# Performance work log

Measured on AMD Instinct MI355X. Metric: run time of the kernel, lower is better.

## Reference

```python
import jax, jax.numpy as jnp
import numpy as np

B, S, E, H = 2, 2048, 1024, 16
D = E // H  # head_dim = 64


def setup_inputs() -> dict:
    key = jax.random.key(0)
    ks = jax.random.split(key, 7)
    scale = 1.0 / np.sqrt(E)
    return {
        "q": jax.random.normal(ks[0], (B, S, E), jnp.float32),
        "k": jax.random.normal(ks[1], (B, S, E), jnp.float32),
        "v": jax.random.normal(ks[2], (B, S, E), jnp.float32),
        "Wq": jax.random.normal(ks[3], (E, E), jnp.float32) * scale,
        "bq": jnp.zeros((E,), jnp.float32),
        "Wk": jax.random.normal(ks[4], (E, E), jnp.float32) * scale,
        "bk": jnp.zeros((E,), jnp.float32),
        "Wv": jax.random.normal(ks[5], (E, E), jnp.float32) * scale,
        "bv": jnp.zeros((E,), jnp.float32),
        "Wo": jax.random.normal(ks[6], (E, E), jnp.float32) * scale,
        "bo": jnp.zeros((E,), jnp.float32),
    }


def _split_heads(x):
    # [B, S, E] -> [B, H, S, D]
    b, s, _ = x.shape
    return x.reshape(b, s, H, D).transpose(0, 2, 1, 3)


def reference(q, k, v, Wq, bq, Wk, bk, Wv, bv, Wo, bo):
    qh = _split_heads(q @ Wq + bq)  # [B,H,S,D]
    kh = _split_heads(k @ Wk + bk)
    vh = _split_heads(v @ Wv + bv)
    scores = jnp.einsum("bhqd,bhkd->bhqk", qh, kh) / jnp.sqrt(jnp.float32(D))
    # causal mask, TF band_part(ones, -1, 0) == lower triangular
    mask = jnp.tril(jnp.ones((S, S), jnp.float32))
    scores = scores * mask - 1e9 * (1.0 - mask)
    weights = jax.nn.softmax(scores, axis=-1)
    attn = jnp.einsum("bhqk,bhkd->bhqd", weights, vh)  # [B,H,S,D]
    concat = attn.transpose(0, 2, 1, 3).reshape(q.shape[0], S, E)
    return concat @ Wo + bo
```

## Files before the change

kernel.cpp:

```cpp
#include <hip/hip_runtime.h>
#include <math.h>

#define Bd 2
#define Sd 2048
#define Ed 1024
#define Hd 16
#define Dd 64
#define Md (Bd * Sd)
#define Kd 1024
#define Nd 1024

typedef __attribute__((ext_vector_type(8))) short bf16x8;
typedef __attribute__((ext_vector_type(4))) float f32x4;

__device__ __forceinline__ unsigned short f2bf(float f) {
    unsigned x = __float_as_uint(f);
    x += 0x7fffu + ((x >> 16) & 1u);
    return (unsigned short)(x >> 16);
}

__device__ __forceinline__ unsigned pk_bf16_rhu(float a, float b) {
    return __builtin_amdgcn_perm(__float_as_uint(b) + 0x8000u,
                                 __float_as_uint(a) + 0x8000u, 0x07060302u);
}

__device__ __forceinline__ void gl2lds16(const unsigned short* g, unsigned short* l) {
    __builtin_amdgcn_global_load_lds(
        (__attribute__((address_space(1))) void*)g,
        (__attribute__((address_space(3))) void*)l, 16, 0, 0);
}

__global__ __launch_bounds__(256) void prep_k(
    const float* __restrict__ q, const float* __restrict__ k, const float* __restrict__ v,
    unsigned short* __restrict__ qb, unsigned short* __restrict__ kb,
    unsigned short* __restrict__ vb,
    const float* __restrict__ w0, const float* __restrict__ w1,
    const float* __restrict__ w2, const float* __restrict__ w3,
    unsigned short* __restrict__ o0, unsigned short* __restrict__ o1,
    unsigned short* __restrict__ o2, unsigned short* __restrict__ o3)
{
    const int bx = blockIdx.x;
    if (bx < 3072) {
        const int zz = bx >> 10;
        const int blk = bx & 1023;
        const float* s = zz == 0 ? q : zz == 1 ? k : v;
        unsigned short* d = zz == 0 ? qb : zz == 1 ? kb : vb;
        const int n4 = (Bd * Sd * Ed) / 4;
        int i = blk * 256 + threadIdx.x;
        for (; i < n4; i += 1024 * 256) {
            float4 x = ((const float4*)s)[i];
            uint2 u = make_uint2(pk_bf16_rhu(x.x, x.y), pk_bf16_rhu(x.z, x.w));
            ((uint2*)d)[i] = u;
        }
        return;
    }
    __shared__ unsigned short Tl[32][36];
    const int idx = bx - 3072;
    const int z   = idx >> 10;
    const int ky  = (idx >> 5) & 31;
    const int nx  = idx & 31;
    const float* W = z == 0 ? w0 : z == 1 ? w1 : z == 2 ? w2 : w3;
    unsigned short* Wt = z == 0 ? o0 : z == 1 ? o1 : z == 2 ? o2 : o3;

    const int t = threadIdx.x;
    const int r = t >> 3;
    const int c4 = (t & 7) * 4;
    const int k0 = ky * 32;
    const int n0 = nx * 32;

    float4 x = *(const float4*)(W + (size_t)(k0 + r) * Nd + n0 + c4);
    Tl[c4 + 0][r] = f2bf(x.x);
    Tl[c4 + 1][r] = f2bf(x.y);
    Tl[c4 + 2][r] = f2bf(x.z);
    Tl[c4 + 3][r] = f2bf(x.w);
    __syncthreads();
    ushort4 u = make_ushort4(Tl[r][c4 + 0], Tl[r][c4 + 1], Tl[r][c4 + 2], Tl[r][c4 + 3]);
    *(ushort4*)(Wt + (size_t)(n0 + r) * Kd + k0 + c4) = u;
}

template <int AM>
__device__ __forceinline__ void gemm_v5(
    const unsigned short* __restrict__ A, const unsigned short* __restrict__ Bt,
    const float* __restrict__ bias, void* __restrict__ Yv,
    int m0, int n0, int mode, float oscale)
{
    constexpr int AMT = AM / 32;
    __shared__ unsigned short As[2][AM * 32];
    __shared__ unsigned short Bs[2][128 * 32];

    const int tid  = threadIdx.x;
    const int w    = tid >> 6;
    const int lane = tid & 63;
    const int ln   = lane & 15;
    const int quad = lane >> 4;
    const int wm = (w >> 1) * (AM / 2);
    const int wn = (w & 1) * 64;

    const int lrow = lane >> 2;
    const int lcol = (lane & 3) * 8;

    const unsigned short* Bg0 = Bt + (size_t)(n0 + (2 * w) * 16 + lrow) * Kd + lcol;
    const unsigned short* Bg1 = Bg0 + 16 * Kd;
    const int aseg = (AM == 128) ? 2 * w : w;
    const unsigned short* Ag0 = A + (size_t)(m0 + aseg * 16 + lrow) * Kd + lcol;
    const unsigned short* Ag1 = Ag0 + 16 * Kd;

    f32x4 acc[AMT][4];
    #pragma unroll
    for (int i = 0; i < AMT; ++i)
        #pragma unroll
        for (int j = 0; j < 4; ++j)
            acc[i][j] = (f32x4){0.f, 0.f, 0.f, 0.f};

    gl2lds16(Bg0, &Bs[0][(2 * w) * 512]);
    gl2lds16(Bg1, &Bs[0][(2 * w) * 512 + 512]);
    gl2lds16(Ag0, &As[0][aseg * 512]);
    if constexpr (AM == 128) gl2lds16(Ag1, &As[0][aseg * 512 + 512]);

    for (int k0 = 0; k0 < Kd; k0 += 32) {
        const int buf = (k0 >> 5) & 1;
        __syncthreads();

        if (k0 + 32 < Kd) {
            gl2lds16(Bg0 + k0 + 32, &Bs[buf ^ 1][(2 * w) * 512]);
            gl2lds16(Bg1 + k0 + 32, &Bs[buf ^ 1][(2 * w) * 512 + 512]);
            gl2lds16(Ag0 + k0 + 32, &As[buf ^ 1][aseg * 512]);
            if constexpr (AM == 128)
                gl2lds16(Ag1 + k0 + 32, &As[buf ^ 1][aseg * 512 + 512]);
        }

        bf16x8 af[AMT], bfr[4];
        #pragma unroll
        for (int mi = 0; mi < AMT; ++mi)
            af[mi] = *(const bf16x8*)(&As[buf][(wm + mi * 16 + ln) * 32 + quad * 8]);
        #pragma unroll
        for (int ni = 0; ni < 4; ++ni)
            bfr[ni] = *(const bf16x8*)(&Bs[buf][(wn + ni * 16 + ln) * 32 + quad * 8]);
        #pragma unroll
        for (int mi = 0; mi < AMT; ++mi)
            #pragma unroll
            for (int ni = 0; ni < 4; ++ni)
                acc[mi][ni] = __builtin_amdgcn_mfma_f32_16x16x32_bf16(
                    af[mi], bfr[ni], acc[mi][ni], 0, 0, 0);
    }

    float bval[4];
    #pragma unroll
    for (int ni = 0; ni < 4; ++ni) bval[ni] = bias[n0 + wn + ni * 16 + ln];

    if (mode == 0) {
        float* Y = (float*)Yv;
        #pragma unroll
        for (int mi = 0; mi < AMT; ++mi) {
            #pragma unroll
            for (int ni = 0; ni < 4; ++ni) {
                int n = n0 + wn + ni * 16 + ln;
                #pragma unroll
                for (int r = 0; r < 4; ++r) {
                    int m = m0 + wm + mi * 16 + quad * 4 + r;
                    Y[(size_t)m * Nd + n] = (acc[mi][ni][r] + bval[ni]) * oscale;
                }
            }
        }
    } else if (mode == 1) {
        unsigned short* Y = (unsigned short*)Yv;
        #pragma unroll
        for (int mi = 0; mi < AMT; ++mi) {
            #pragma unroll
            for (int ni = 0; ni < 4; ++ni) {
                int n = n0 + wn + ni * 16 + ln;
                int h = n >> 6, d = n & 63;
                #pragma unroll
                for (int r = 0; r < 4; ++r) {
                    int m = m0 + wm + mi * 16 + quad * 4 + r;
                    int b = m >> 11, s = m & 2047;
                    Y[(((size_t)b * Hd + h) * Sd + s) * Dd + d] =
                        f2bf((acc[mi][ni][r] + bval[ni]) * oscale);
                }
            }
        }
    } else {
        unsigned short* Y = (unsigned short*)Yv;
        #pragma unroll
        for (int mi = 0; mi < AMT; ++mi) {
            int mbase = m0 + wm + mi * 16 + quad * 4;
            int b = mbase >> 11, s = mbase & 2047;
            #pragma unroll
            for (int ni = 0; ni < 4; ++ni) {
                int n = n0 + wn + ni * 16 + ln;
                int h = n >> 6, d = n & 63;
                ushort4 u = make_ushort4(
                    f2bf((acc[mi][ni][0] + bval[ni]) * oscale),
                    f2bf((acc[mi][ni][1] + bval[ni]) * oscale),
                    f2bf((acc[mi][ni][2] + bval[ni]) * oscale),
                    f2bf((acc[mi][ni][3] + bval[ni]) * oscale));
                *(ushort4*)(Y + (((size_t)b * Hd + h) * Dd + d) * Sd + s) = u;
            }
        }
    }
}

__global__ __launch_bounds__(256) void proj_gemm_k(
    const unsigned short* A0, const unsigned short* A1, const unsigned short* A2,
    const unsigned short* B0, const unsigned short* B1, const unsigned short* B2,
    const float* b0, const float* b1, const float* b2,
    unsigned short* Y0, unsigned short* Y1, unsigned short* Y2)
{
    const int l    = blockIdx.x;
    const int xcd  = l & 7;
    const int g    = l >> 3;
    const int n_t  = g & 7;
    const int msub = (g >> 3) & 3;
    const int z    = g >> 5;
    const int m_t  = xcd * 4 + msub;

    const unsigned short* A = z == 0 ? A0 : z == 1 ? A1 : A2;
    const unsigned short* B = z == 0 ? B0 : z == 1 ? B1 : B2;
    const float* bias       = z == 0 ? b0 : z == 1 ? b1 : b2;
    unsigned short* Y       = z == 0 ? Y0 : z == 1 ? Y1 : Y2;
    gemm_v5<128>(A, B, bias, Y, m_t * 128, n_t * 128,
                 z == 2 ? 2 : 1,
                 z == 0 ? 0.18033688011112042f : 1.0f);
}

__global__ __launch_bounds__(256) void out_gemm_k(
    const unsigned short* A, const unsigned short* Bt, const float* bias, float* Y)
{
    const int l    = blockIdx.x;
    const int xcd  = l & 7;
    const int g    = l >> 3;
    const int n_t  = g & 7;
    const int msub = g >> 3;
    const int m_t  = xcd * 8 + msub;
    gemm_v5<64>(A, Bt, bias, Y, m_t * 64, n_t * 128, 0, 1.0f);
}

__global__ __launch_bounds__(256) void attn_mfma_k(
    const unsigned short* __restrict__ Qg,
    const unsigned short* __restrict__ Kg,
    const unsigned short* __restrict__ Vg,
    unsigned short* __restrict__ Aout)
{
    __shared__ unsigned short Ks[2][2][64 * 64];
    __shared__ unsigned short Vs[2][2][64 * 64];
    __shared__ unsigned short Pt[4][16][72];

    const int tid  = threadIdx.x;
    const int w    = tid >> 6;
    const int lane = tid & 63;
    const int ln   = lane & 15;
    const int quad = lane >> 4;

    const int l   = blockIdx.x;
    const int bh  = (l & 7) * 4 + ((l >> 3) & 3);
    const int qtA = l >> 5;
    const int qtB = 31 - qtA;
    const int b   = bh >> 4;
    const int h   = bh & 15;

    const size_t baseQK = (size_t)bh * Sd * Dd;
    const size_t baseV  = (size_t)bh * Dd * Sd;
    const f32x4 vzero = {0.f, 0.f, 0.f, 0.f};

    const int nsub = qtB + 1;
    const int ngrp = (nsub + 1) >> 1;

    const int sr = lane >> 3;
    const int sc = ((lane & 7) ^ sr) * 8;
    const int rb0 = w * 16, rb1 = w * 16 + 8;
    const int swl = ln & 7;
    const int c0 = ((quad    ) ^ swl) * 8;
    const int c1 = ((quad + 4) ^ swl) * 8;

    const int qrowA = qtA * 64 + w * 16;
    const int qrowB = qtB * 64 + w * 16;
    const int qgA = qrowA + ln, qgB = qrowB + ln;
    const unsigned short* qpA = Qg + baseQK + (size_t)qgA * Dd + 8 * quad;
    const unsigned short* qpB = Qg + baseQK + (size_t)qgB * Dd + 8 * quad;
    const bf16x8 qA0 = *(const bf16x8*)(qpA), qA1 = *(const bf16x8*)(qpA + 32);
    const bf16x8 qB0 = *(const bf16x8*)(qpB), qB1 = *(const bf16x8*)(qpB + 32);

    float lA = 0.f, lB = 0.f;
    f32x4 OA[4], OB[4];
    #pragma unroll
    for (int t = 0; t < 4; ++t) { OA[t] = vzero; OB[t] = vzero; }

    const unsigned short* Kst0 = Kg + baseQK + (size_t)(rb0 + sr) * Dd + sc;
    const unsigned short* Kst1 = Kg + baseQK + (size_t)(rb1 + sr) * Dd + sc;
    const unsigned short* Vst0 = Vg + baseV  + (size_t)(rb0 + sr) * Sd + sc;
    const unsigned short* Vst1 = Vg + baseV  + (size_t)(rb1 + sr) * Sd + sc;

    #pragma unroll
    for (int s = 0; s < 2; ++s) {
        const int nk = s * 64;
        gl2lds16(Kst0 + (size_t)nk * Dd, &Ks[0][s][rb0 * 64]);
        gl2lds16(Kst1 + (size_t)nk * Dd, &Ks[0][s][rb1 * 64]);
        gl2lds16(Vst0 + nk, &Vs[0][s][rb0 * 64]);
        gl2lds16(Vst1 + nk, &Vs[0][s][rb1 * 64]);
    }

    for (int g = 0; g < ngrp; ++g) {
        const int cur = g & 1;
        __syncthreads();

        if (g + 1 < ngrp) {
            #pragma unroll
            for (int s = 0; s < 2; ++s) {
                const int ts = 2 * (g + 1) + s;
                if (ts < nsub) {
                    const int nk = ts * 64;
                    gl2lds16(Kst0 + (size_t)nk * Dd, &Ks[cur ^ 1][s][rb0 * 64]);
                    gl2lds16(Kst1 + (size_t)nk * Dd, &Ks[cur ^ 1][s][rb1 * 64]);
                    gl2lds16(Vst0 + nk, &Vs[cur ^ 1][s][rb0 * 64]);
                    gl2lds16(Vst1 + nk, &Vs[cur ^ 1][s][rb1 * 64]);
                }
            }
        }

        #pragma unroll
        for (int s = 0; s < 2; ++s) {
            const int it = 2 * g + s;
            if (it >= nsub) break;
            const int nk  = it * 64;
            const bool doA = (it <= qtA);

            bf16x8 kf0[4], kf1[4];
            #pragma unroll
            for (int t = 0; t < 4; ++t) {
                const int R = (t * 16 + ln) * 64;
                kf0[t] = *(const bf16x8*)&Ks[cur][s][R + c0];
                kf1[t] = *(const bf16x8*)&Ks[cur][s][R + c1];
            }

            f32x4 SB[4], SA[4];
            #pragma unroll
            for (int t = 0; t < 4; ++t) {
                f32x4 z = __builtin_amdgcn_mfma_f32_16x16x32_bf16(kf0[t], qB0, vzero, 0, 0, 0);
                SB[t]   = __builtin_amdgcn_mfma_f32_16x16x32_bf16(kf1[t], qB1, z,     0, 0, 0);
            }
            if (doA) {
                #pragma unroll
                for (int t = 0; t < 4; ++t) {
                    f32x4 z = __builtin_amdgcn_mfma_f32_16x16x32_bf16(kf0[t], qA0, vzero, 0, 0, 0);
                    SA[t]   = __builtin_amdgcn_mfma_f32_16x16x32_bf16(kf1[t], qA1, z,     0, 0, 0);
                }
            }

            if (it == qtB) {
                #pragma unroll
                for (int t = 0; t < 4; ++t)
                    #pragma unroll
                    for (int r = 0; r < 4; ++r)
                        if (nk + t * 16 + quad * 4 + r > qgB)
                            SB[t][r] = -1e30f;
            }
            if (doA && it == qtA) {
                #pragma unroll
                for (int t = 0; t < 4; ++t)
                    #pragma unroll
                    for (int r = 0; r < 4; ++r)
                        if (nk + t * 16 + quad * 4 + r > qgA)
                            SA[t][r] = -1e30f;
            }

            {
                float p[16]; float rsum = 0.f;
                #pragma unroll
                for (int t = 0; t < 4; ++t)
                    #pragma unroll
                    for (int r = 0; r < 4; ++r) {
                        float e = __builtin_amdgcn_exp2f(SB[t][r]);
                        p[t * 4 + r] = e; rsum += e;
                    }
                lB += rsum;
                #pragma unroll
                for (int t = 0; t < 4; ++t) {
                    uint2 u = make_uint2(pk_bf16_rhu(p[t * 4 + 0], p[t * 4 + 1]),
                                         pk_bf16_rhu(p[t * 4 + 2], p[t * 4 + 3]));
                    *(uint2*)&Pt[w][ln][t * 16 + quad * 4] = u;
                }
            }
            const bf16x8 pfB0 = *(const bf16x8*)&Pt[w][ln][8 * quad];
            const bf16x8 pfB1 = *(const bf16x8*)&Pt[w][ln][32 + 8 * quad];

            bf16x8 pfA0, pfA1;
            if (doA) {
                float p[16]; float rsum = 0.f;
                #pragma unroll
                for (int t = 0; t < 4; ++t)
                    #pragma unroll
                    for (int r = 0; r < 4; ++r) {
                        float e = __builtin_amdgcn_exp2f(SA[t][r]);
                        p[t * 4 + r] = e; rsum += e;
                    }
                lA += rsum;
                #pragma unroll
                for (int t = 0; t < 4; ++t) {
                    uint2 u = make_uint2(pk_bf16_rhu(p[t * 4 + 0], p[t * 4 + 1]),
                                         pk_bf16_rhu(p[t * 4 + 2], p[t * 4 + 3]));
                    *(uint2*)&Pt[w][ln][t * 16 + quad * 4] = u;
                }
                pfA0 = *(const bf16x8*)&Pt[w][ln][8 * quad];
                pfA1 = *(const bf16x8*)&Pt[w][ln][32 + 8 * quad];
            }

            #pragma unroll
            for (int t = 0; t < 4; ++t) {
                const int R = (t * 16 + ln) * 64;
                bf16x8 v0 = *(const bf16x8*)&Vs[cur][s][R + c0];
                bf16x8 v1 = *(const bf16x8*)&Vs[cur][s][R + c1];
                OB[t] = __builtin_amdgcn_mfma_f32_16x16x32_bf16(v0, pfB0, OB[t], 0, 0, 0);
                OB[t] = __builtin_amdgcn_mfma_f32_16x16x32_bf16(v1, pfB1, OB[t], 0, 0, 0);
                if (doA) {
                    OA[t] = __builtin_amdgcn_mfma_f32_16x16x32_bf16(v0, pfA0, OA[t], 0, 0, 0);
                    OA[t] = __builtin_amdgcn_mfma_f32_16x16x32_bf16(v1, pfA1, OA[t], 0, 0, 0);
                }
            }

            if (doA && it == qtA) {
                float l_run = lA;
                l_run += __shfl_xor(l_run, 16);
                l_run += __shfl_xor(l_run, 32);
                float inv = 1.f / l_run;
                unsigned short* op =
                    Aout + ((size_t)b * Sd + qgA) * Ed + h * 64 + quad * 4;
                #pragma unroll
                for (int t = 0; t < 4; ++t) {
                    ushort4 u = make_ushort4(f2bf(OA[t][0] * inv), f2bf(OA[t][1] * inv),
                                             f2bf(OA[t][2] * inv), f2bf(OA[t][3] * inv));
                    *(ushort4*)(op + t * 16) = u;
                }
            }
        }
    }

    float l_run = lB;
    l_run += __shfl_xor(l_run, 16);
    l_run += __shfl_xor(l_run, 32);
    float inv = 1.f / l_run;
    unsigned short* op = Aout + ((size_t)b * Sd + qgB) * Ed + h * 64 + quad * 4;
    #pragma unroll
    for (int t = 0; t < 4; ++t) {
        ushort4 u = make_ushort4(f2bf(OB[t][0] * inv), f2bf(OB[t][1] * inv),
                                 f2bf(OB[t][2] * inv), f2bf(OB[t][3] * inv));
        *(ushort4*)(op + t * 16) = u;
    }
}

extern "C" void kernel_launch(void* const* d_in, const int* in_sizes, int n_in,
                              void* d_out, int out_size, void* d_ws, size_t ws_size,
                              hipStream_t stream) {
    const float* q  = (const float*)d_in[0];
    const float* k  = (const float*)d_in[1];
    const float* v  = (const float*)d_in[2];
    const float* Wq = (const float*)d_in[3];
    const float* bq = (const float*)d_in[4];
    const float* Wk = (const float*)d_in[5];
    const float* bk = (const float*)d_in[6];
    const float* Wv = (const float*)d_in[7];
    const float* bv = (const float*)d_in[8];
    const float* Wo = (const float*)d_in[9];
    const float* bo = (const float*)d_in[10];

    const size_t TENS = (size_t)Bd * Sd * Ed;
    const size_t WE   = (size_t)Ed * Ed;
    unsigned short* qb  = (unsigned short*)d_ws;
    unsigned short* kb  = qb + TENS;
    unsigned short* vb  = kb + TENS;
    unsigned short* Wqt = vb + TENS;
    unsigned short* Wkt = Wqt + WE;
    unsigned short* Wvt = Wkt + WE;
    unsigned short* Wot = Wvt + WE;
    unsigned short* Qh  = Wot + WE;
    unsigned short* Kh  = Qh + TENS;
    unsigned short* Vt  = Kh + TENS;
    unsigned short* An  = Vt + TENS;

    prep_k<<<dim3(7168), 256, 0, stream>>>(q, k, v, qb, kb, vb,
                                           Wq, Wk, Wv, Wo, Wqt, Wkt, Wvt, Wot);
    proj_gemm_k<<<dim3(768), 256, 0, stream>>>(
        qb, kb, vb, Wqt, Wkt, Wvt, bq, bk, bv, Qh, Kh, Vt);
    attn_mfma_k<<<dim3(512), 256, 0, stream>>>(Qh, Kh, Vt, An);
    out_gemm_k<<<dim3(512), 256, 0, stream>>>(An, Wot, bo, (float*)d_out);
}
```

Before: 208.0 us.

## Split attention KV sub-tiles across two wave groups with LDS merge

```diff
diff --git a/kernel.cpp b/kernel.cpp
--- a/kernel.cpp
+++ b/kernel.cpp
@@ -235,18 +235,21 @@
     gemm_v5<64>(A, Bt, bias, Y, m_t * 64, n_t * 128, 0, 1.0f);
 }
 
-__global__ __launch_bounds__(256) void attn_mfma_k(
+__global__ __launch_bounds__(512, 4) void attn_mfma_k(
     const unsigned short* __restrict__ Qg,
     const unsigned short* __restrict__ Kg,
     const unsigned short* __restrict__ Vg,
     unsigned short* __restrict__ Aout)
 {
-    __shared__ unsigned short Ks[2][2][64 * 64];
-    __shared__ unsigned short Vs[2][2][64 * 64];
-    __shared__ unsigned short Pt[4][16][72];
+    __shared__ unsigned short lds_all[40960];
+    unsigned short* Ksb = lds_all;
+    unsigned short* Vsb = lds_all + 16384;
+    unsigned short* Ptb = lds_all + 32768;
 
     const int tid  = threadIdx.x;
-    const int w    = tid >> 6;
+    const int w8   = tid >> 6;
+    const int grp  = w8 >> 2;
+    const int w    = w8 & 3;
     const int lane = tid & 63;
     const int ln   = lane & 15;
     const int quad = lane >> 4;
@@ -265,12 +268,13 @@
     const int nsub = qtB + 1;
     const int ngrp = (nsub + 1) >> 1;
 
+    const int rw = w8 * 8;
     const int sr = lane >> 3;
     const int sc = ((lane & 7) ^ sr) * 8;
-    const int rb0 = w * 16, rb1 = w * 16 + 8;
     const int swl = ln & 7;
     const int c0 = ((quad    ) ^ swl) * 8;
     const int c1 = ((quad + 4) ^ swl) * 8;
+    const int pswz = swl << 3;
 
     const int qrowA = qtA * 64 + w * 16;
     const int qrowB = qtB * 64 + w * 16;
@@ -285,18 +289,15 @@
     #pragma unroll
     for (int t = 0; t < 4; ++t) { OA[t] = vzero; OB[t] = vzero; }
 
-    const unsigned short* Kst0 = Kg + baseQK + (size_t)(rb0 + sr) * Dd + sc;
-    const unsigned short* Kst1 = Kg + baseQK + (size_t)(rb1 + sr) * Dd + sc;
-    const unsigned short* Vst0 = Vg + baseV  + (size_t)(rb0 + sr) * Sd + sc;
-    const unsigned short* Vst1 = Vg + baseV  + (size_t)(rb1 + sr) * Sd + sc;
+    const unsigned short* Kst = Kg + baseQK + (size_t)(rw + sr) * Dd + sc;
+    const unsigned short* Vst = Vg + baseV  + (size_t)(rw + sr) * Sd + sc;
+    unsigned short* Ptw = Ptb + (w8 * 16 + ln) * 64;
 
     #pragma unroll
     for (int s = 0; s < 2; ++s) {
         const int nk = s * 64;
-        gl2lds16(Kst0 + (size_t)nk * Dd, &Ks[0][s][rb0 * 64]);
-        gl2lds16(Kst1 + (size_t)nk * Dd, &Ks[0][s][rb1 * 64]);
-        gl2lds16(Vst0 + nk, &Vs[0][s][rb0 * 64]);
-        gl2lds16(Vst1 + nk, &Vs[0][s][rb1 * 64]);
+        gl2lds16(Kst + (size_t)nk * Dd, Ksb + s * 4096 + rw * 64);
+        gl2lds16(Vst + nk,              Vsb + s * 4096 + rw * 64);
     }
 
     for (int g = 0; g < ngrp; ++g) {
@@ -309,27 +310,27 @@
                 const int ts = 2 * (g + 1) + s;
                 if (ts < nsub) {
                     const int nk = ts * 64;
-                    gl2lds16(Kst0 + (size_t)nk * Dd, &Ks[cur ^ 1][s][rb0 * 64]);
-                    gl2lds16(Kst1 + (size_t)nk * Dd, &Ks[cur ^ 1][s][rb1 * 64]);
-                    gl2lds16(Vst0 + nk, &Vs[cur ^ 1][s][rb0 * 64]);
-                    gl2lds16(Vst1 + nk, &Vs[cur ^ 1][s][rb1 * 64]);
-                }
-            }
-        }
-
-        #pragma unroll
-        for (int s = 0; s < 2; ++s) {
-            const int it = 2 * g + s;
-            if (it >= nsub) break;
+                    gl2lds16(Kst + (size_t)nk * Dd,
+                             Ksb + ((cur ^ 1) * 2 + s) * 4096 + rw * 64);
+                    gl2lds16(Vst + nk,
+                             Vsb + ((cur ^ 1) * 2 + s) * 4096 + rw * 64);
+                }
+            }
+        }
+
+        const int it = 2 * g + grp;
+        if (it < nsub) {
             const int nk  = it * 64;
             const bool doA = (it <= qtA);
+            const unsigned short* Kc = Ksb + (cur * 2 + grp) * 4096;
+            const unsigned short* Vc = Vsb + (cur * 2 + grp) * 4096;
 
             bf16x8 kf0[4], kf1[4];
             #pragma unroll
             for (int t = 0; t < 4; ++t) {
                 const int R = (t * 16 + ln) * 64;
-                kf0[t] = *(const bf16x8*)&Ks[cur][s][R + c0];
-                kf1[t] = *(const bf16x8*)&Ks[cur][s][R + c1];
+                kf0[t] = *(const bf16x8*)&Kc[R + c0];
+                kf1[t] = *(const bf16x8*)&Kc[R + c1];
             }
 
             f32x4 SB[4], SA[4];
@@ -377,11 +378,11 @@
                 for (int t = 0; t < 4; ++t) {
                     uint2 u = make_uint2(pk_bf16_rhu(p[t * 4 + 0], p[t * 4 + 1]),
                                          pk_bf16_rhu(p[t * 4 + 2], p[t * 4 + 3]));
-                    *(uint2*)&Pt[w][ln][t * 16 + quad * 4] = u;
-                }
-            }
-            const bf16x8 pfB0 = *(const bf16x8*)&Pt[w][ln][8 * quad];
-            const bf16x8 pfB1 = *(const bf16x8*)&Pt[w][ln][32 + 8 * quad];
+                    *(uint2*)&Ptw[(t * 16 + quad * 4) ^ pswz] = u;
+                }
+            }
+            const bf16x8 pfB0 = *(const bf16x8*)&Ptw[(8 * quad) ^ pswz];
+            const bf16x8 pfB1 = *(const bf16x8*)&Ptw[(32 + 8 * quad) ^ pswz];
 
             bf16x8 pfA0, pfA1;
             if (doA) {
@@ -398,17 +399,17 @@
                 for (int t = 0; t < 4; ++t) {
                     uint2 u = make_uint2(pk_bf16_rhu(p[t * 4 + 0], p[t * 4 + 1]),
                                          pk_bf16_rhu(p[t * 4 + 2], p[t * 4 + 3]));
-                    *(uint2*)&Pt[w][ln][t * 16 + quad * 4] = u;
-                }
-                pfA0 = *(const bf16x8*)&Pt[w][ln][8 * quad];
-                pfA1 = *(const bf16x8*)&Pt[w][ln][32 + 8 * quad];
+                    *(uint2*)&Ptw[(t * 16 + quad * 4) ^ pswz] = u;
+                }
+                pfA0 = *(const bf16x8*)&Ptw[(8 * quad) ^ pswz];
+                pfA1 = *(const bf16x8*)&Ptw[(32 + 8 * quad) ^ pswz];
             }
 
             #pragma unroll
             for (int t = 0; t < 4; ++t) {
                 const int R = (t * 16 + ln) * 64;
-                bf16x8 v0 = *(const bf16x8*)&Vs[cur][s][R + c0];
-                bf16x8 v1 = *(const bf16x8*)&Vs[cur][s][R + c1];
+                bf16x8 v0 = *(const bf16x8*)&Vc[R + c0];
+                bf16x8 v1 = *(const bf16x8*)&Vc[R + c1];
                 OB[t] = __builtin_amdgcn_mfma_f32_16x16x32_bf16(v0, pfB0, OB[t], 0, 0, 0);
                 OB[t] = __builtin_amdgcn_mfma_f32_16x16x32_bf16(v1, pfB1, OB[t], 0, 0, 0);
                 if (doA) {
@@ -416,34 +417,54 @@
                     OA[t] = __builtin_amdgcn_mfma_f32_16x16x32_bf16(v1, pfA1, OA[t], 0, 0, 0);
                 }
             }
-
-            if (doA && it == qtA) {
-                float l_run = lA;
-                l_run += __shfl_xor(l_run, 16);
-                l_run += __shfl_xor(l_run, 32);
-                float inv = 1.f / l_run;
-                unsigned short* op =
-                    Aout + ((size_t)b * Sd + qgA) * Ed + h * 64 + quad * 4;
-                #pragma unroll
-                for (int t = 0; t < 4; ++t) {
-                    ushort4 u = make_ushort4(f2bf(OA[t][0] * inv), f2bf(OA[t][1] * inv),
-                                             f2bf(OA[t][2] * inv), f2bf(OA[t][3] * inv));
-                    *(ushort4*)(op + t * 16) = u;
-                }
-            }
-        }
-    }
-
-    float l_run = lB;
-    l_run += __shfl_xor(l_run, 16);
-    l_run += __shfl_xor(l_run, 32);
-    float inv = 1.f / l_run;
-    unsigned short* op = Aout + ((size_t)b * Sd + qgB) * Ed + h * 64 + quad * 4;
-    #pragma unroll
-    for (int t = 0; t < 4; ++t) {
-        ushort4 u = make_ushort4(f2bf(OB[t][0] * inv), f2bf(OB[t][1] * inv),
-                                 f2bf(OB[t][2] * inv), f2bf(OB[t][3] * inv));
-        *(ushort4*)(op + t * 16) = u;
+        }
+    }
+
+    __syncthreads();
+    float* mrg = (float*)lds_all;
+    const int slot = (w * 64 + lane) * 36;
+    if (grp == 1) {
+        #pragma unroll
+        for (int t = 0; t < 4; ++t) {
+            *(f32x4*)&mrg[slot + t * 4]      = OA[t];
+            *(f32x4*)&mrg[slot + 16 + t * 4] = OB[t];
+        }
+        mrg[slot + 32] = lA;
+        mrg[slot + 33] = lB;
+    }
+    __syncthreads();
+    if (grp == 0) {
+        #pragma unroll
+        for (int t = 0; t < 4; ++t) {
+            OA[t] += *(const f32x4*)&mrg[slot + t * 4];
+            OB[t] += *(const f32x4*)&mrg[slot + 16 + t * 4];
+        }
+        lA += mrg[slot + 32];
+        lB += mrg[slot + 33];
+
+        float lrA = lA;
+        lrA += __shfl_xor(lrA, 16);
+        lrA += __shfl_xor(lrA, 32);
+        float invA = 1.f / lrA;
+        unsigned short* opA = Aout + ((size_t)b * Sd + qgA) * Ed + h * 64 + quad * 4;
+        #pragma unroll
+        for (int t = 0; t < 4; ++t) {
+            ushort4 u = make_ushort4(f2bf(OA[t][0] * invA), f2bf(OA[t][1] * invA),
+                                     f2bf(OA[t][2] * invA), f2bf(OA[t][3] * invA));
+            *(ushort4*)(opA + t * 16) = u;
+        }
+
+        float lrB = lB;
+        lrB += __shfl_xor(lrB, 16);
+        lrB += __shfl_xor(lrB, 32);
+        float invB = 1.f / lrB;
+        unsigned short* opB = Aout + ((size_t)b * Sd + qgB) * Ed + h * 64 + quad * 4;
+        #pragma unroll
+        for (int t = 0; t < 4; ++t) {
+            ushort4 u = make_ushort4(f2bf(OB[t][0] * invB), f2bf(OB[t][1] * invB),
+                                     f2bf(OB[t][2] * invB), f2bf(OB[t][3] * invB));
+            *(ushort4*)(opB + t * 16) = u;
+        }
     }
 }
 
@@ -480,6 +501,6 @@
                                            Wq, Wk, Wv, Wo, Wqt, Wkt, Wvt, Wot);
     proj_gemm_k<<<dim3(768), 256, 0, stream>>>(
         qb, kb, vb, Wqt, Wkt, Wvt, bq, bk, bv, Qh, Kh, Vt);
-    attn_mfma_k<<<dim3(512), 256, 0, stream>>>(Qh, Kh, Vt, An);
+    attn_mfma_k<<<dim3(512), 512, 0, stream>>>(Qh, Kh, Vt, An);
     out_gemm_k<<<dim3(512), 256, 0, stream>>>(An, Wot, bo, (float*)d_out);
 }
```

Measured after the change: 224.4 us. +7.9%, slower.
